# Optimization experiments

Measured on AMD Instinct MI355X. Metric: run time of the kernel, lower is better.

The kernel has to match this reference:

```python
import jax, jax.numpy as jnp
import numpy as np

# Dimensions (see shape_source): 192x192 images, 10 MC samples, 4 classes (3 fg), batch 16
B, S, CLS, H, W = 16, 10, 4, 192, 192
FG = CLS - 1
FSCALE = 3   # neighbor-count kernel
CSCALE = 3   # constraint-reward kernel
K = float(CSCALE * CSCALE)


def setup_inputs() -> dict:
    key = jax.random.key(0)
    k1, k2 = jax.random.split(key)
    logits = jax.random.normal(k1, (B, CLS, H, W), dtype=jnp.float32)
    preds = jax.nn.softmax(logits, axis=1)          # per-pixel class probabilities
    samples = jax.random.randint(k2, (B, S, H, W), 0, CLS, dtype=jnp.int32)  # sampled label maps
    return {"preds": preds, "samples": samples}


def _conv_ones(x, ksize):
    # x: [N, H, W]; all-ones ksize x ksize conv, SAME padding (== pad (k-1)/2 in torch)
    kern = jnp.ones((1, 1, ksize, ksize), x.dtype)
    y = jax.lax.conv_general_dilated(x[:, None], kern, (1, 1), 'SAME')
    return y[:, 0]


def _dilate8(m):
    # 3x3 max-pool == one step of 8-connectivity dilation (skimage full connectivity)
    return jax.lax.reduce_window(m, 0.0, jax.lax.max, (3, 3), (1, 1), 'SAME')


def _flood(fg, seed):
    # connected component of fg containing flat index `seed` (8-connectivity),
    # equivalent to skimage.flood_fill from the seed followed by == new_value
    m0 = jnp.zeros(fg.size, fg.dtype).at[seed].set(1.0).reshape(fg.shape) * fg
    def cond(st):
        return st[1]
    def body(st):
        m, _ = st
        d = _dilate8(m) * fg
        return d, jnp.any(d != m)
    m, _ = jax.lax.while_loop(cond, body, (m0, jnp.array(True)))
    return m


def _connectivity_rewards(samples):
    # samples: [B, S, H, W] int class maps -> rewards [B, S, H, W]
    cls_ids = jnp.arange(1, CLS)
    fg = (samples[:, :, None] == cls_ids[None, None, :, None, None]).astype(jnp.float32)  # [B,S,FG,H,W]
    fgf = fg.reshape(-1, H, W)                     # [B*S*FG, H, W]
    nb = _conv_ones(fgf, FSCALE) * fgf             # foreground neighbor counts
    seeds = jnp.argmax(nb.reshape(nb.shape[0], -1), axis=1)  # seed = max-neighbor pixel (first max)
    comp = jax.vmap(_flood)(fgf, seeds)            # largest-seeded connected component
    fc = _conv_ones(comp, CSCALE) * comp           # F_fg_neigbors
    reward = fc / K                                # soft reward
    per_c = reward - (fgf - comp)                  # + isolation penalty: -(fg - fill_connect)
    return per_c.reshape(B, S, FG, H, W).sum(axis=2)


def reference(preds, samples):
    rewards = _connectivity_rewards(samples)       # [B,S,H,W], constant wrt preds
    # prob of the sampled class at each pixel: preds[b, samples[b,s,h,w], h, w]
    probs = jnp.take_along_axis(
        jnp.broadcast_to(preds[:, None], (B, S, CLS, H, W)),
        samples[:, :, None].astype(jnp.int32), axis=2)[:, :, 0]
    # REINFORCE-style constraint loss: maximize reward-weighted log-prob
    loss = -(jnp.log(probs + 1e-8) * rewards).mean()
    return loss
```

## Files before the change

kernel.cpp:

```cpp
#include <hip/hip_runtime.h>
#include <stdint.h>

#define BB 16
#define SS 10
#define CLSN 4
#define FGN 3
#define HH 192
#define WW 192
#define NPIX (HH * WW)
#define WPR 3
#define NWORDS (HH * WPR)
#define NT 512
#define NW 8
#define CH (NWORDS / NW)

typedef unsigned long long u64;

#define FAD(a, b, c, s, cy)            \
    do {                               \
        u64 t_ = (a) ^ (b);            \
        (s) = t_ ^ (c);                \
        (cy) = ((a) & (b)) | (t_ & (c)); \
    } while (0)

#define SMEAR3(u0, u1, u2, s0, s1, s2)                          \
    do {                                                        \
        (s0) = (u0) | ((u0) << 1) | ((u0) >> 1) | ((u1) << 63); \
        (s1) = (u1) | ((u1) << 1) | ((u0) >> 63) | ((u1) >> 1) | ((u2) << 63); \
        (s2) = (u2) | ((u2) << 1) | ((u1) >> 63) | ((u2) >> 1); \
    } while (0)

__device__ __forceinline__ void plane9(const u64* bd, int k,
                                       u64& P0, u64& P1, u64& P2, u64& P3, u64& mid)
{
    const int r = k / WPR;
    const int wc = k - r * WPR;
    u64 rows[3][3];
#pragma unroll
    for (int di = 0; di < 3; ++di) {
        int rr = r + di - 1;
#pragma unroll
        for (int dj = 0; dj < 3; ++dj) {
            int ww = wc + dj - 1;
            rows[di][dj] = (rr >= 0 && rr < HH && ww >= 0 && ww < WPR)
                           ? bd[rr * WPR + ww] : 0ULL;
        }
    }
    mid = rows[1][1];
    u64 in[9];
#pragma unroll
    for (int i = 0; i < 3; ++i) {
        u64 m = rows[i][1], lf = rows[i][0], rg = rows[i][2];
        in[3 * i + 0] = m;
        in[3 * i + 1] = (m << 1) | (lf >> 63);
        in[3 * i + 2] = (m >> 1) | (rg << 63);
    }
    u64 s0a, c0a, s0b, c0b, s0c, c0c, c0d, s1a, c1a, c1b;
    FAD(in[0], in[1], in[2], s0a, c0a);
    FAD(in[3], in[4], in[5], s0b, c0b);
    FAD(in[6], in[7], in[8], s0c, c0c);
    FAD(s0a, s0b, s0c, P0, c0d);
    FAD(c0a, c0b, c0c, s1a, c1a);
    P1 = s1a ^ c0d;
    c1b = s1a & c0d;
    P2 = c1a ^ c1b;
    P3 = c1a & c1b;
}

__global__ __launch_bounds__(NT) void cc_loss_kernel(
    const float* __restrict__ preds,
    const int* __restrict__ samples,
    double* __restrict__ acc)
{
    __shared__ u64 fgw[NWORDS];
    __shared__ u64 compB[NWORDS];
    __shared__ unsigned int wkey[NW];
    __shared__ double wsum[NW];
    __shared__ unsigned int seedIdx;

    const int blk = blockIdx.x;
    const int c = 1 + blk / (BB * SS);
    const int pair = blk % (BB * SS);
    const int b = pair / SS;
    const int s = pair % SS;

    const int tid  = threadIdx.x;
    const int lane = tid & 63;
    const int wv   = tid >> 6;

    const int* smp = samples + (size_t)pair * NPIX;
    const float* pp = preds + ((size_t)b * CLSN + c) * NPIX;

    float facc = 0.0f;

    {
        const int base = wv * CH;
        for (int i = 0; i < CH; i += 6) {
            int v[6]; float pv[6];
#pragma unroll
            for (int j = 0; j < 6; ++j) {
                int pix = ((base + i + j) << 6) + lane;
                v[j]  = smp[pix];
                pv[j] = pp[pix];
            }
#pragma unroll
            for (int j = 0; j < 6; ++j) {
                u64 m = __ballot(v[j] == c);
                if (lane == 0) fgw[base + i + j] = m;
                float lp = __logf(pv[j] + 1e-8f);
                facc -= (v[j] == c) ? lp : 0.0f;
            }
        }
    }
    __syncthreads();

    {
        unsigned int bestkey = 0u;
        for (int k = tid; k < NWORDS; k += NT) {
            u64 P0, P1, P2, P3, mid;
            plane9(fgw, k, P0, P1, P2, P3, mid);
            if (mid) {
                u64 cand = mid, t;
                unsigned v = 0;
                t = cand & P3; if (t) { cand = t; v |= 8u; }
                t = cand & P2; if (t) { cand = t; v |= 4u; }
                t = cand & P1; if (t) { cand = t; v |= 2u; }
                t = cand & P0; if (t) { cand = t; v |= 1u; }
                unsigned pix = ((unsigned)k << 6) + (unsigned)(__ffsll(cand) - 1);
                unsigned key = (v << 16) | (36863u - pix);
                if (key > bestkey) bestkey = key;
            }
        }
#pragma unroll
        for (int off = 32; off > 0; off >>= 1) {
            unsigned int o = (unsigned int)__shfl_xor((int)bestkey, off, 64);
            if (o > bestkey) bestkey = o;
        }
        if (lane == 0) wkey[wv] = bestkey;
    }
    __syncthreads();
    if (tid == 0) {
        unsigned int kk = 0u;
#pragma unroll
        for (int i = 0; i < NW; ++i)
            if (wkey[i] > kk) kk = wkey[i];
        seedIdx = 36863u - (kk & 0xFFFFu);
    }
    __syncthreads();

    if (wv == 0) {
        const unsigned seed = seedIdx;
        u64 f[3][3], cc[3][3];
        const int rbase = 3 * lane;
#pragma unroll
        for (int j = 0; j < 3; ++j)
#pragma unroll
            for (int w = 0; w < 3; ++w) {
                f[j][w] = fgw[(rbase + j) * WPR + w];
                cc[j][w] = 0ULL;
            }
        {
            const int sr = seed / WW, sw = (seed % WW) >> 6, sb = seed & 63;
            if (sr / 3 == lane)
                cc[sr % 3][sw] = (1ULL << sb) & f[sr % 3][sw];
        }
        for (;;) {
            u64 bA0 = __shfl_up(cc[2][0], 1, 64);
            u64 bA1 = __shfl_up(cc[2][1], 1, 64);
            u64 bA2 = __shfl_up(cc[2][2], 1, 64);
            u64 tB0 = __shfl_down(cc[0][0], 1, 64);
            u64 tB1 = __shfl_down(cc[0][1], 1, 64);
            u64 tB2 = __shfl_down(cc[0][2], 1, 64);
            if (lane == 0)  { bA0 = bA1 = bA2 = 0ULL; }
            if (lane == 63) { tB0 = tB1 = tB2 = 0ULL; }

            u64 o00 = cc[0][0], o01 = cc[0][1], o02 = cc[0][2];
            u64 o10 = cc[1][0], o11 = cc[1][1], o12 = cc[1][2];
            u64 o20 = cc[2][0], o21 = cc[2][1], o22 = cc[2][2];

            u64 u0, u1, u2, s0, s1, s2;
            u0 = bA0 | cc[0][0] | cc[1][0]; u1 = bA1 | cc[0][1] | cc[1][1]; u2 = bA2 | cc[0][2] | cc[1][2];
            SMEAR3(u0, u1, u2, s0, s1, s2);
            cc[0][0] = s0 & f[0][0]; cc[0][1] = s1 & f[0][1]; cc[0][2] = s2 & f[0][2];

            u0 = cc[0][0] | cc[1][0] | cc[2][0]; u1 = cc[0][1] | cc[1][1] | cc[2][1]; u2 = cc[0][2] | cc[1][2] | cc[2][2];
            SMEAR3(u0, u1, u2, s0, s1, s2);
            cc[1][0] = s0 & f[1][0]; cc[1][1] = s1 & f[1][1]; cc[1][2] = s2 & f[1][2];

            u0 = cc[1][0] | cc[2][0] | tB0; u1 = cc[1][1] | cc[2][1] | tB1; u2 = cc[1][2] | cc[2][2] | tB2;
            SMEAR3(u0, u1, u2, s0, s1, s2);
            cc[2][0] = s0 & f[2][0]; cc[2][1] = s1 & f[2][1]; cc[2][2] = s2 & f[2][2];

            u0 = cc[0][0] | cc[1][0] | cc[2][0]; u1 = cc[0][1] | cc[1][1] | cc[2][1]; u2 = cc[0][2] | cc[1][2] | cc[2][2];
            SMEAR3(u0, u1, u2, s0, s1, s2);
            cc[1][0] = s0 & f[1][0]; cc[1][1] = s1 & f[1][1]; cc[1][2] = s2 & f[1][2];

            u0 = bA0 | cc[0][0] | cc[1][0]; u1 = bA1 | cc[0][1] | cc[1][1]; u2 = bA2 | cc[0][2] | cc[1][2];
            SMEAR3(u0, u1, u2, s0, s1, s2);
            cc[0][0] = s0 & f[0][0]; cc[0][1] = s1 & f[0][1]; cc[0][2] = s2 & f[0][2];

            u64 d = (cc[0][0] ^ o00) | (cc[0][1] ^ o01) | (cc[0][2] ^ o02)
                  | (cc[1][0] ^ o10) | (cc[1][1] ^ o11) | (cc[1][2] ^ o12)
                  | (cc[2][0] ^ o20) | (cc[2][1] ^ o21) | (cc[2][2] ^ o22);
            if (!__any(d != 0ULL)) break;
        }
#pragma unroll
        for (int j = 0; j < 3; ++j)
#pragma unroll
            for (int w = 0; w < 3; ++w)
                compB[(rbase + j) * WPR + w] = cc[j][w];
    }
    __syncthreads();

    {
        const int base = wv * CH;
        for (int k = base; k < base + CH; ++k) {
            u64 cw = compB[k];
            if (cw == 0ULL) continue;
            u64 P0, P1, P2, P3, mid;
            plane9(compB, k, P0, P1, P2, P3, mid);
            if ((cw >> lane) & 1ULL) {
                int cnt = (int)((P0 >> lane) & 1ULL)
                        | ((int)((P1 >> lane) & 1ULL) << 1)
                        | ((int)((P2 >> lane) & 1ULL) << 2)
                        | ((int)((P3 >> lane) & 1ULL) << 3);
                float lp = __logf(pp[(k << 6) + lane] + 1e-8f);
                facc += ((float)cnt * (1.0f / 9.0f) + 1.0f) * lp;
            }
        }
    }

#pragma unroll
    for (int off = 32; off > 0; off >>= 1)
        facc += __shfl_xor(facc, off, 64);
    if (lane == 0) wsum[wv] = (double)facc;
    __syncthreads();
    if (tid == 0) {
        double t = 0.0;
#pragma unroll
        for (int i = 0; i < NW; ++i) t += wsum[i];
        atomicAdd(acc, t);
    }
}

__global__ void finalize_kernel(const double* __restrict__ acc, float* __restrict__ out)
{
    if (threadIdx.x == 0 && blockIdx.x == 0)
        out[0] = (float)(-acc[0] / (double)((long long)BB * SS * NPIX));
}

extern "C" void kernel_launch(void* const* d_in, const int* in_sizes, int n_in,
                              void* d_out, int out_size, void* d_ws, size_t ws_size,
                              hipStream_t stream)
{
    const float* preds   = (const float*)d_in[0];
    const int*   samples = (const int*)d_in[1];
    double* acc = (double*)d_ws;

    hipMemsetAsync(acc, 0, sizeof(double), stream);
    hipLaunchKernelGGL(cc_loss_kernel, dim3(BB * SS * FGN), dim3(NT), 0, stream,
                       preds, samples, acc);
    hipLaunchKernelGGL(finalize_kernel, dim3(1), dim3(64), 0, stream,
                       acc, (float*)d_out);
}
```

Measured before the change: 51.19 us.

## Split into dense bitmask pass and single-wave component kernel

Splits the fused kernel into two. The first is a dense pass that reads each sample once, writes foreground bitmasks for all three classes to workspace, and accumulates the -log p term. The second runs one 64-thread block per task to pick the seed, flood-fill, and score only the nonzero component words. This removes the threefold re-read of samples and the idle waves during the serial flood fill, at the cost of a global round-trip for the bitmasks and an extra launch. It falls back to the old fused kernel if the workspace is too small.

Result: slower. 85.88 us (+67.8%).

```diff
diff --git a/kernel.cpp b/kernel.cpp
--- a/kernel.cpp
+++ b/kernel.cpp
@@ -10,9 +10,13 @@
 #define NPIX (HH * WW)
 #define WPR 3
 #define NWORDS (HH * WPR)
-#define NT 512
-#define NW 8
-#define CH (NWORDS / NW)
+#define NPAIR (BB * SS)
+#define NTASK (NPAIR * FGN)
+
+#define K1_BLOCKS 1440
+#define K1_THREADS 256
+#define K1_WAVES (K1_BLOCKS * 4)
+#define K1_CHUNK ((NPAIR * NWORDS) / K1_WAVES)
 
 typedef unsigned long long u64;
 
@@ -67,22 +71,199 @@
     P3 = c1a & c1b;
 }
 
-__global__ __launch_bounds__(NT) void cc_loss_kernel(
+__global__ __launch_bounds__(K1_THREADS) void k1_dense(
+    const float* __restrict__ preds,
+    const int* __restrict__ samples,
+    u64* __restrict__ fgAll,
+    double* __restrict__ acc)
+{
+    __shared__ double wsum[4];
+    const int tid  = threadIdx.x;
+    const int lane = tid & 63;
+    const int wv   = tid >> 6;
+    const int wid  = blockIdx.x * 4 + wv;
+
+    float facc = 0.0f;
+    const int base = wid * K1_CHUNK;
+#pragma unroll 4
+    for (int i = 0; i < K1_CHUNK; ++i) {
+        const int t = base + i;
+        const int pair = t / NWORDS;
+        const int word = t - pair * NWORDS;
+        const int b = pair / SS;
+        const int pix = (word << 6) + lane;
+        const int v = samples[(size_t)pair * NPIX + pix];
+        const float p = preds[((size_t)b * CLSN + v) * NPIX + pix];
+        u64 m1 = __ballot(v == 1);
+        u64 m2 = __ballot(v == 2);
+        u64 m3 = __ballot(v == 3);
+        if (lane == 0) {
+            fgAll[(size_t)(0 * NPAIR + pair) * NWORDS + word] = m1;
+            fgAll[(size_t)(1 * NPAIR + pair) * NWORDS + word] = m2;
+            fgAll[(size_t)(2 * NPAIR + pair) * NWORDS + word] = m3;
+        }
+        float lp = __logf(p + 1e-8f);
+        facc -= (v > 0) ? lp : 0.0f;
+    }
+#pragma unroll
+    for (int off = 32; off > 0; off >>= 1)
+        facc += __shfl_xor(facc, off, 64);
+    if (lane == 0) wsum[wv] = (double)facc;
+    __syncthreads();
+    if (tid == 0)
+        atomicAdd(acc, wsum[0] + wsum[1] + wsum[2] + wsum[3]);
+}
+
+__global__ __launch_bounds__(64) void k2_comp(
+    const float* __restrict__ preds,
+    const u64* __restrict__ fgAll,
+    double* __restrict__ acc)
+{
+    __shared__ u64 fgw[NWORDS];
+    __shared__ u64 cmp[NWORDS];
+
+    const int blk  = blockIdx.x;
+    const int c    = 1 + blk / NPAIR;
+    const int pair = blk % NPAIR;
+    const int b    = pair / SS;
+    const int lane = threadIdx.x;
+
+    const u64* fgsrc = fgAll + (size_t)blk * NWORDS;
+#pragma unroll
+    for (int i = 0; i < 9; ++i)
+        fgw[lane + 64 * i] = fgsrc[lane + 64 * i];
+    __syncthreads();
+
+    unsigned int bestkey = 0u;
+#pragma unroll
+    for (int i = 0; i < 9; ++i) {
+        const int k = lane + 64 * i;
+        u64 P0, P1, P2, P3, mid;
+        plane9(fgw, k, P0, P1, P2, P3, mid);
+        if (mid) {
+            u64 cand = mid, t;
+            unsigned v = 0;
+            t = cand & P3; if (t) { cand = t; v |= 8u; }
+            t = cand & P2; if (t) { cand = t; v |= 4u; }
+            t = cand & P1; if (t) { cand = t; v |= 2u; }
+            t = cand & P0; if (t) { cand = t; v |= 1u; }
+            unsigned pix = ((unsigned)k << 6) + (unsigned)(__ffsll(cand) - 1);
+            unsigned key = (v << 16) | (36863u - pix);
+            if (key > bestkey) bestkey = key;
+        }
+    }
+#pragma unroll
+    for (int off = 32; off > 0; off >>= 1) {
+        unsigned int o = (unsigned int)__shfl_xor((int)bestkey, off, 64);
+        if (o > bestkey) bestkey = o;
+    }
+    const unsigned seed = 36863u - (bestkey & 0xFFFFu);
+
+    u64 f[3][3], cc[3][3];
+#pragma unroll
+    for (int j = 0; j < 3; ++j)
+#pragma unroll
+        for (int w = 0; w < 3; ++w) {
+            f[j][w] = fgw[(3 * lane + j) * WPR + w];
+            cc[j][w] = 0ULL;
+        }
+    {
+        const int sr = (int)(seed / WW), sw = ((int)seed % WW) >> 6, sb = (int)seed & 63;
+        if (sr / 3 == lane)
+            cc[sr % 3][sw] = (1ULL << sb) & f[sr % 3][sw];
+    }
+    for (;;) {
+        u64 bA0 = __shfl_up(cc[2][0], 1, 64);
+        u64 bA1 = __shfl_up(cc[2][1], 1, 64);
+        u64 bA2 = __shfl_up(cc[2][2], 1, 64);
+        u64 tB0 = __shfl_down(cc[0][0], 1, 64);
+        u64 tB1 = __shfl_down(cc[0][1], 1, 64);
+        u64 tB2 = __shfl_down(cc[0][2], 1, 64);
+        if (lane == 0)  { bA0 = bA1 = bA2 = 0ULL; }
+        if (lane == 63) { tB0 = tB1 = tB2 = 0ULL; }
+
+        u64 o00 = cc[0][0], o01 = cc[0][1], o02 = cc[0][2];
+        u64 o10 = cc[1][0], o11 = cc[1][1], o12 = cc[1][2];
+        u64 o20 = cc[2][0], o21 = cc[2][1], o22 = cc[2][2];
+
+        u64 u0, u1, u2, s0, s1, s2;
+        u0 = bA0 | cc[0][0] | cc[1][0]; u1 = bA1 | cc[0][1] | cc[1][1]; u2 = bA2 | cc[0][2] | cc[1][2];
+        SMEAR3(u0, u1, u2, s0, s1, s2);
+        cc[0][0] = s0 & f[0][0]; cc[0][1] = s1 & f[0][1]; cc[0][2] = s2 & f[0][2];
+
+        u0 = cc[0][0] | cc[1][0] | cc[2][0]; u1 = cc[0][1] | cc[1][1] | cc[2][1]; u2 = cc[0][2] | cc[1][2] | cc[2][2];
+        SMEAR3(u0, u1, u2, s0, s1, s2);
+        cc[1][0] = s0 & f[1][0]; cc[1][1] = s1 & f[1][1]; cc[1][2] = s2 & f[1][2];
+
+        u0 = cc[1][0] | cc[2][0] | tB0; u1 = cc[1][1] | cc[2][1] | tB1; u2 = cc[1][2] | cc[2][2] | tB2;
+        SMEAR3(u0, u1, u2, s0, s1, s2);
+        cc[2][0] = s0 & f[2][0]; cc[2][1] = s1 & f[2][1]; cc[2][2] = s2 & f[2][2];
+
+        u0 = cc[0][0] | cc[1][0] | cc[2][0]; u1 = cc[0][1] | cc[1][1] | cc[2][1]; u2 = cc[0][2] | cc[1][2] | cc[2][2];
+        SMEAR3(u0, u1, u2, s0, s1, s2);
+        cc[1][0] = s0 & f[1][0]; cc[1][1] = s1 & f[1][1]; cc[1][2] = s2 & f[1][2];
+
+        u0 = bA0 | cc[0][0] | cc[1][0]; u1 = bA1 | cc[0][1] | cc[1][1]; u2 = bA2 | cc[0][2] | cc[1][2];
+        SMEAR3(u0, u1, u2, s0, s1, s2);
+        cc[0][0] = s0 & f[0][0]; cc[0][1] = s1 & f[0][1]; cc[0][2] = s2 & f[0][2];
+
+        u64 d = (cc[0][0] ^ o00) | (cc[0][1] ^ o01) | (cc[0][2] ^ o02)
+              | (cc[1][0] ^ o10) | (cc[1][1] ^ o11) | (cc[1][2] ^ o12)
+              | (cc[2][0] ^ o20) | (cc[2][1] ^ o21) | (cc[2][2] ^ o22);
+        if (!__any(d != 0ULL)) break;
+    }
+
+#pragma unroll
+    for (int j = 0; j < 3; ++j)
+#pragma unroll
+        for (int w = 0; w < 3; ++w)
+            cmp[(3 * lane + j) * WPR + w] = cc[j][w];
+    __syncthreads();
+
+    float facc = 0.0f;
+    const float* pp = preds + ((size_t)b * CLSN + c) * NPIX;
+#pragma unroll
+    for (int jw = 0; jw < 9; ++jw) {
+        const int j = jw / 3, w = jw - 3 * (jw / 3);
+        u64 m = __ballot(cc[j][w] != 0ULL);
+        while (m) {
+            const int src = (int)(__ffsll(m) - 1);
+            m &= m - 1;
+            const int k = 9 * src + jw;
+            u64 P0, P1, P2, P3, mid;
+            plane9(cmp, k, P0, P1, P2, P3, mid);
+            if ((mid >> lane) & 1ULL) {
+                int cnt = (int)((P0 >> lane) & 1ULL)
+                        | ((int)((P1 >> lane) & 1ULL) << 1)
+                        | ((int)((P2 >> lane) & 1ULL) << 2)
+                        | ((int)((P3 >> lane) & 1ULL) << 3);
+                float lp = __logf(pp[(k << 6) + lane] + 1e-8f);
+                facc += ((float)cnt * (1.0f / 9.0f) + 1.0f) * lp;
+            }
+        }
+    }
+#pragma unroll
+    for (int off = 32; off > 0; off >>= 1)
+        facc += __shfl_xor(facc, off, 64);
+    if (lane == 0)
+        atomicAdd(acc, (double)facc);
+}
+
+__global__ __launch_bounds__(512) void cc_loss_fused(
     const float* __restrict__ preds,
     const int* __restrict__ samples,
     double* __restrict__ acc)
 {
     __shared__ u64 fgw[NWORDS];
     __shared__ u64 compB[NWORDS];
-    __shared__ unsigned int wkey[NW];
-    __shared__ double wsum[NW];
+    __shared__ unsigned int wkey[8];
+    __shared__ double wsum[8];
     __shared__ unsigned int seedIdx;
 
     const int blk = blockIdx.x;
-    const int c = 1 + blk / (BB * SS);
-    const int pair = blk % (BB * SS);
+    const int c = 1 + blk / NPAIR;
+    const int pair = blk % NPAIR;
     const int b = pair / SS;
-    const int s = pair % SS;
 
     const int tid  = threadIdx.x;
     const int lane = tid & 63;
@@ -92,10 +273,9 @@
     const float* pp = preds + ((size_t)b * CLSN + c) * NPIX;
 
     float facc = 0.0f;
-
     {
-        const int base = wv * CH;
-        for (int i = 0; i < CH; i += 6) {
+        const int base = wv * 72;
+        for (int i = 0; i < 72; i += 6) {
             int v[6]; float pv[6];
 #pragma unroll
             for (int j = 0; j < 6; ++j) {
@@ -113,10 +293,9 @@
         }
     }
     __syncthreads();
-
     {
         unsigned int bestkey = 0u;
-        for (int k = tid; k < NWORDS; k += NT) {
+        for (int k = tid; k < NWORDS; k += 512) {
             u64 P0, P1, P2, P3, mid;
             plane9(fgw, k, P0, P1, P2, P3, mid);
             if (mid) {
@@ -142,12 +321,11 @@
     if (tid == 0) {
         unsigned int kk = 0u;
 #pragma unroll
-        for (int i = 0; i < NW; ++i)
+        for (int i = 0; i < 8; ++i)
             if (wkey[i] > kk) kk = wkey[i];
         seedIdx = 36863u - (kk & 0xFFFFu);
     }
     __syncthreads();
-
     if (wv == 0) {
         const unsigned seed = seedIdx;
         u64 f[3][3], cc[3][3];
@@ -173,32 +351,25 @@
             u64 tB2 = __shfl_down(cc[0][2], 1, 64);
             if (lane == 0)  { bA0 = bA1 = bA2 = 0ULL; }
             if (lane == 63) { tB0 = tB1 = tB2 = 0ULL; }
-
             u64 o00 = cc[0][0], o01 = cc[0][1], o02 = cc[0][2];
             u64 o10 = cc[1][0], o11 = cc[1][1], o12 = cc[1][2];
             u64 o20 = cc[2][0], o21 = cc[2][1], o22 = cc[2][2];
-
             u64 u0, u1, u2, s0, s1, s2;
             u0 = bA0 | cc[0][0] | cc[1][0]; u1 = bA1 | cc[0][1] | cc[1][1]; u2 = bA2 | cc[0][2] | cc[1][2];
             SMEAR3(u0, u1, u2, s0, s1, s2);
             cc[0][0] = s0 & f[0][0]; cc[0][1] = s1 & f[0][1]; cc[0][2] = s2 & f[0][2];
-
             u0 = cc[0][0] | cc[1][0] | cc[2][0]; u1 = cc[0][1] | cc[1][1] | cc[2][1]; u2 = cc[0][2] | cc[1][2] | cc[2][2];
             SMEAR3(u0, u1, u2, s0, s1, s2);
             cc[1][0] = s0 & f[1][0]; cc[1][1] = s1 & f[1][1]; cc[1][2] = s2 & f[1][2];
-
             u0 = cc[1][0] | cc[2][0] | tB0; u1 = cc[1][1] | cc[2][1] | tB1; u2 = cc[1][2] | cc[2][2] | tB2;
             SMEAR3(u0, u1, u2, s0, s1, s2);
             cc[2][0] = s0 & f[2][0]; cc[2][1] = s1 & f[2][1]; cc[2][2] = s2 & f[2][2];
-
             u0 = cc[0][0] | cc[1][0] | cc[2][0]; u1 = cc[0][1] | cc[1][1] | cc[2][1]; u2 = cc[0][2] | cc[1][2] | cc[2][2];
             SMEAR3(u0, u1, u2, s0, s1, s2);
             cc[1][0] = s0 & f[1][0]; cc[1][1] = s1 & f[1][1]; cc[1][2] = s2 & f[1][2];
-
             u0 = bA0 | cc[0][0] | cc[1][0]; u1 = bA1 | cc[0][1] | cc[1][1]; u2 = bA2 | cc[0][2] | cc[1][2];
             SMEAR3(u0, u1, u2, s0, s1, s2);
             cc[0][0] = s0 & f[0][0]; cc[0][1] = s1 & f[0][1]; cc[0][2] = s2 & f[0][2];
-
             u64 d = (cc[0][0] ^ o00) | (cc[0][1] ^ o01) | (cc[0][2] ^ o02)
                   | (cc[1][0] ^ o10) | (cc[1][1] ^ o11) | (cc[1][2] ^ o12)
                   | (cc[2][0] ^ o20) | (cc[2][1] ^ o21) | (cc[2][2] ^ o22);
@@ -211,10 +382,9 @@
                 compB[(rbase + j) * WPR + w] = cc[j][w];
     }
     __syncthreads();
-
     {
-        const int base = wv * CH;
-        for (int k = base; k < base + CH; ++k) {
+        const int base = wv * 72;
+        for (int k = base; k < base + 72; ++k) {
             u64 cw = compB[k];
             if (cw == 0ULL) continue;
             u64 P0, P1, P2, P3, mid;
@@ -229,7 +399,6 @@
             }
         }
     }
-
 #pragma unroll
     for (int off = 32; off > 0; off >>= 1)
         facc += __shfl_xor(facc, off, 64);
@@ -238,7 +407,7 @@
     if (tid == 0) {
         double t = 0.0;
 #pragma unroll
-        for (int i = 0; i < NW; ++i) t += wsum[i];
+        for (int i = 0; i < 8; ++i) t += wsum[i];
         atomicAdd(acc, t);
     }
 }
@@ -255,11 +424,24 @@
 {
     const float* preds   = (const float*)d_in[0];
     const int*   samples = (const int*)d_in[1];
-    double* acc = (double*)d_ws;
-
-    hipMemsetAsync(acc, 0, sizeof(double), stream);
-    hipLaunchKernelGGL(cc_loss_kernel, dim3(BB * SS * FGN), dim3(NT), 0, stream,
-                       preds, samples, acc);
-    hipLaunchKernelGGL(finalize_kernel, dim3(1), dim3(64), 0, stream,
-                       acc, (float*)d_out);
-}
+
+    const size_t fg_bytes = (size_t)NTASK * NWORDS * sizeof(u64);
+    if (ws_size >= fg_bytes + sizeof(double)) {
+        u64* fgAll  = (u64*)d_ws;
+        double* acc = (double*)((char*)d_ws + fg_bytes);
+        hipMemsetAsync(acc, 0, sizeof(double), stream);
+        hipLaunchKernelGGL(k1_dense, dim3(K1_BLOCKS), dim3(K1_THREADS), 0, stream,
+                           preds, samples, fgAll, acc);
+        hipLaunchKernelGGL(k2_comp, dim3(NTASK), dim3(64), 0, stream,
+                           preds, fgAll, acc);
+        hipLaunchKernelGGL(finalize_kernel, dim3(1), dim3(64), 0, stream,
+                           acc, (float*)d_out);
+    } else {
+        double* acc = (double*)d_ws;
+        hipMemsetAsync(acc, 0, sizeof(double), stream);
+        hipLaunchKernelGGL(cc_loss_fused, dim3(NTASK), dim3(512), 0, stream,
+                           preds, samples, acc);
+        hipLaunchKernelGGL(finalize_kernel, dim3(1), dim3(64), 0, stream,
+                           acc, (float*)d_out);
+    }
+}
```

## Vectorize mask build, double-step flood rows, compact nonzero component words

Applied to the files above, without the earlier changes.

Each thread now loads 16 contiguous pixels with int4/float4 loads and packs a 16-bit mask directly into shared memory, replacing the per-word ballots. The block size drops from 512 to 256 threads. Each flood-fill row step now smears twice per iteration so the fill converges in fewer loop iterations. The reward pass first compacts the nonzero component words into a list with shared atomics and then prefetches the next word's probabilities while computing the current one. Fewer threads per block means less parallelism for the load phase, and the compaction adds an extra synchronisation.

New measurement: 49.35 us. -3.6%, faster.

```diff
diff --git a/kernel.cpp b/kernel.cpp
--- a/kernel.cpp
+++ b/kernel.cpp
@@ -10,11 +10,13 @@
 #define NPIX (HH * WW)
 #define WPR 3
 #define NWORDS (HH * WPR)
-#define NT 512
-#define NW 8
-#define CH (NWORDS / NW)
+#define NPAIR (BB * SS)
+#define NTASK (NPAIR * FGN)
+#define NT 256
+#define NW 4
 
 typedef unsigned long long u64;
+typedef unsigned short u16;
 
 #define FAD(a, b, c, s, cy)            \
     do {                               \
@@ -67,55 +69,71 @@
     P3 = c1a & c1b;
 }
 
-__global__ __launch_bounds__(NT) void cc_loss_kernel(
+__global__ __launch_bounds__(NT) void cc_fused(
     const float* __restrict__ preds,
     const int* __restrict__ samples,
     double* __restrict__ acc)
 {
     __shared__ u64 fgw[NWORDS];
-    __shared__ u64 compB[NWORDS];
-    __shared__ unsigned int wkey[NW];
+    __shared__ u64 cmp[NWORDS];
+    __shared__ unsigned wkey[NW];
     __shared__ double wsum[NW];
-    __shared__ unsigned int seedIdx;
+    __shared__ unsigned seedSh;
+    __shared__ int cntSh;
+    __shared__ short wlist[NWORDS];
 
     const int blk = blockIdx.x;
-    const int c = 1 + blk / (BB * SS);
-    const int pair = blk % (BB * SS);
+    const int c = 1 + blk / NPAIR;
+    const int pair = blk % NPAIR;
     const int b = pair / SS;
-    const int s = pair % SS;
 
     const int tid  = threadIdx.x;
     const int lane = tid & 63;
     const int wv   = tid >> 6;
 
-    const int* smp = samples + (size_t)pair * NPIX;
-    const float* pp = preds + ((size_t)b * CLSN + c) * NPIX;
+    const int* __restrict__ smp  = samples + (size_t)pair * NPIX;
+    const float* __restrict__ pp = preds + ((size_t)b * CLSN + c) * NPIX;
+
+    if (tid == 0) cntSh = 0;
 
     float facc = 0.0f;
 
     {
-        const int base = wv * CH;
-        for (int i = 0; i < CH; i += 6) {
-            int v[6]; float pv[6];
-#pragma unroll
-            for (int j = 0; j < 6; ++j) {
-                int pix = ((base + i + j) << 6) + lane;
-                v[j]  = smp[pix];
-                pv[j] = pp[pix];
-            }
-#pragma unroll
-            for (int j = 0; j < 6; ++j) {
-                u64 m = __ballot(v[j] == c);
-                if (lane == 0) fgw[base + i + j] = m;
-                float lp = __logf(pv[j] + 1e-8f);
-                facc -= (v[j] == c) ? lp : 0.0f;
-            }
+        u16* nib = (u16*)fgw;
+        for (int sc = 0; sc < 9; ++sc) {
+            const int ci = sc * NT + tid;
+            const int px = ci << 4;
+            const int4 v0 = *(const int4*)(smp + px);
+            const int4 v1 = *(const int4*)(smp + px + 4);
+            const int4 v2 = *(const int4*)(smp + px + 8);
+            const int4 v3 = *(const int4*)(smp + px + 12);
+            const float4 q0 = *(const float4*)(pp + px);
+            const float4 q1 = *(const float4*)(pp + px + 4);
+            const float4 q2 = *(const float4*)(pp + px + 8);
+            const float4 q3 = *(const float4*)(pp + px + 12);
+            unsigned m = 0u;
+#define ACC1(vv, qq, sh)                                              \
+            {                                                          \
+                const bool hit_ = ((vv) == c);                         \
+                m |= ((unsigned)hit_) << (sh);                         \
+                facc -= hit_ ? __logf((qq) + 1e-8f) : 0.0f;            \
+            }
+            ACC1(v0.x, q0.x, 0)  ACC1(v0.y, q0.y, 1)
+            ACC1(v0.z, q0.z, 2)  ACC1(v0.w, q0.w, 3)
+            ACC1(v1.x, q1.x, 4)  ACC1(v1.y, q1.y, 5)
+            ACC1(v1.z, q1.z, 6)  ACC1(v1.w, q1.w, 7)
+            ACC1(v2.x, q2.x, 8)  ACC1(v2.y, q2.y, 9)
+            ACC1(v2.z, q2.z, 10) ACC1(v2.w, q2.w, 11)
+            ACC1(v3.x, q3.x, 12) ACC1(v3.y, q3.y, 13)
+            ACC1(v3.z, q3.z, 14) ACC1(v3.w, q3.w, 15)
+#undef ACC1
+            nib[ci] = (u16)m;
         }
     }
     __syncthreads();
 
     {
-        unsigned int bestkey = 0u;
+        unsigned bestkey = 0u;
         for (int k = tid; k < NWORDS; k += NT) {
             u64 P0, P1, P2, P3, mid;
             plane9(fgw, k, P0, P1, P2, P3, mid);
@@ -133,23 +151,23 @@
         }
 #pragma unroll
         for (int off = 32; off > 0; off >>= 1) {
-            unsigned int o = (unsigned int)__shfl_xor((int)bestkey, off, 64);
+            unsigned o = (unsigned)__shfl_xor((int)bestkey, off, 64);
             if (o > bestkey) bestkey = o;
         }
         if (lane == 0) wkey[wv] = bestkey;
     }
     __syncthreads();
     if (tid == 0) {
-        unsigned int kk = 0u;
-#pragma unroll
-        for (int i = 0; i < NW; ++i)
-            if (wkey[i] > kk) kk = wkey[i];
-        seedIdx = 36863u - (kk & 0xFFFFu);
+        unsigned kk = wkey[0];
+        if (wkey[1] > kk) kk = wkey[1];
+        if (wkey[2] > kk) kk = wkey[2];
+        if (wkey[3] > kk) kk = wkey[3];
+        seedSh = 36863u - (kk & 0xFFFFu);
     }
     __syncthreads();
 
     if (wv == 0) {
-        const unsigned seed = seedIdx;
+        const unsigned seed = seedSh;
         u64 f[3][3], cc[3][3];
         const int rbase = 3 * lane;
 #pragma unroll
@@ -160,7 +178,7 @@
                 cc[j][w] = 0ULL;
             }
         {
-            const int sr = seed / WW, sw = (seed % WW) >> 6, sb = seed & 63;
+            const int sr = (int)(seed / WW), sw = ((int)seed % WW) >> 6, sb = (int)seed & 63;
             if (sr / 3 == lane)
                 cc[sr % 3][sw] = (1ULL << sb) & f[sr % 3][sw];
         }
@@ -178,26 +196,25 @@
             u64 o10 = cc[1][0], o11 = cc[1][1], o12 = cc[1][2];
             u64 o20 = cc[2][0], o21 = cc[2][1], o22 = cc[2][2];
 
-            u64 u0, u1, u2, s0, s1, s2;
-            u0 = bA0 | cc[0][0] | cc[1][0]; u1 = bA1 | cc[0][1] | cc[1][1]; u2 = bA2 | cc[0][2] | cc[1][2];
-            SMEAR3(u0, u1, u2, s0, s1, s2);
-            cc[0][0] = s0 & f[0][0]; cc[0][1] = s1 & f[0][1]; cc[0][2] = s2 & f[0][2];
-
-            u0 = cc[0][0] | cc[1][0] | cc[2][0]; u1 = cc[0][1] | cc[1][1] | cc[2][1]; u2 = cc[0][2] | cc[1][2] | cc[2][2];
-            SMEAR3(u0, u1, u2, s0, s1, s2);
-            cc[1][0] = s0 & f[1][0]; cc[1][1] = s1 & f[1][1]; cc[1][2] = s2 & f[1][2];
-
-            u0 = cc[1][0] | cc[2][0] | tB0; u1 = cc[1][1] | cc[2][1] | tB1; u2 = cc[1][2] | cc[2][2] | tB2;
-            SMEAR3(u0, u1, u2, s0, s1, s2);
-            cc[2][0] = s0 & f[2][0]; cc[2][1] = s1 & f[2][1]; cc[2][2] = s2 & f[2][2];
-
-            u0 = cc[0][0] | cc[1][0] | cc[2][0]; u1 = cc[0][1] | cc[1][1] | cc[2][1]; u2 = cc[0][2] | cc[1][2] | cc[2][2];
-            SMEAR3(u0, u1, u2, s0, s1, s2);
-            cc[1][0] = s0 & f[1][0]; cc[1][1] = s1 & f[1][1]; cc[1][2] = s2 & f[1][2];
-
-            u0 = bA0 | cc[0][0] | cc[1][0]; u1 = bA1 | cc[0][1] | cc[1][1]; u2 = bA2 | cc[0][2] | cc[1][2];
-            SMEAR3(u0, u1, u2, s0, s1, s2);
-            cc[0][0] = s0 & f[0][0]; cc[0][1] = s1 & f[0][1]; cc[0][2] = s2 & f[0][2];
+#define RSTEP(A0, A1, A2, B0, B1, B2, C0, C1, C2, J)                          \
+            {                                                                  \
+                u64 u0 = (A0) | (B0) | (C0);                                   \
+                u64 u1 = (A1) | (B1) | (C1);                                   \
+                u64 u2 = (A2) | (B2) | (C2);                                   \
+                u64 t0, t1, t2, s0, s1, s2;                                    \
+                SMEAR3(u0, u1, u2, t0, t1, t2);                                \
+                t0 &= f[J][0]; t1 &= f[J][1]; t2 &= f[J][2];                   \
+                SMEAR3(t0, t1, t2, s0, s1, s2);                                \
+                cc[J][0] = s0 & f[J][0];                                       \
+                cc[J][1] = s1 & f[J][1];                                       \
+                cc[J][2] = s2 & f[J][2];                                       \
+            }
+            RSTEP(bA0, bA1, bA2, cc[0][0], cc[0][1], cc[0][2], cc[1][0], cc[1][1], cc[1][2], 0)
+            RSTEP(cc[0][0], cc[0][1], cc[0][2], cc[1][0], cc[1][1], cc[1][2], cc[2][0], cc[2][1], cc[2][2], 1)
+            RSTEP(cc[1][0], cc[1][1], cc[1][2], cc[2][0], cc[2][1], cc[2][2], tB0, tB1, tB2, 2)
+            RSTEP(cc[0][0], cc[0][1], cc[0][2], cc[1][0], cc[1][1], cc[1][2], cc[2][0], cc[2][1], cc[2][2], 1)
+            RSTEP(bA0, bA1, bA2, cc[0][0], cc[0][1], cc[0][2], cc[1][0], cc[1][1], cc[1][2], 0)
+#undef RSTEP
 
             u64 d = (cc[0][0] ^ o00) | (cc[0][1] ^ o01) | (cc[0][2] ^ o02)
                   | (cc[1][0] ^ o10) | (cc[1][1] ^ o11) | (cc[1][2] ^ o12)
@@ -208,25 +225,34 @@
         for (int j = 0; j < 3; ++j)
 #pragma unroll
             for (int w = 0; w < 3; ++w)
-                compB[(rbase + j) * WPR + w] = cc[j][w];
-    }
-    __syncthreads();
-
+                cmp[(rbase + j) * WPR + w] = cc[j][w];
+    }
+    __syncthreads();
+
+    for (int k = tid; k < NWORDS; k += NT)
+        if (cmp[k] != 0ULL) { int idx = atomicAdd(&cntSh, 1); wlist[idx] = (short)k; }
+    __syncthreads();
     {
-        const int base = wv * CH;
-        for (int k = base; k < base + CH; ++k) {
-            u64 cw = compB[k];
-            if (cw == 0ULL) continue;
+        const int n = cntSh;
+        int i = wv;
+        int kc = (i < n) ? (int)wlist[i] : -1;
+        float pc = 0.0f;
+        if (kc >= 0) pc = pp[(kc << 6) + lane];
+        while (kc >= 0) {
+            const int i2 = i + NW;
+            const int k2 = (i2 < n) ? (int)wlist[i2] : -1;
+            float p2 = 0.0f;
+            if (k2 >= 0) p2 = pp[(k2 << 6) + lane];
             u64 P0, P1, P2, P3, mid;
-            plane9(compB, k, P0, P1, P2, P3, mid);
-            if ((cw >> lane) & 1ULL) {
-                int cnt = (int)((P0 >> lane) & 1ULL)
-                        | ((int)((P1 >> lane) & 1ULL) << 1)
-                        | ((int)((P2 >> lane) & 1ULL) << 2)
-                        | ((int)((P3 >> lane) & 1ULL) << 3);
-                float lp = __logf(pp[(k << 6) + lane] + 1e-8f);
-                facc += ((float)cnt * (1.0f / 9.0f) + 1.0f) * lp;
-            }
+            plane9(cmp, kc, P0, P1, P2, P3, mid);
+            if ((mid >> lane) & 1ULL) {
+                int ct = (int)((P0 >> lane) & 1ULL)
+                       | ((int)((P1 >> lane) & 1ULL) << 1)
+                       | ((int)((P2 >> lane) & 1ULL) << 2)
+                       | ((int)((P3 >> lane) & 1ULL) << 3);
+                facc += ((float)ct * (1.0f / 9.0f) + 1.0f) * __logf(pc + 1e-8f);
+            }
+            i = i2; kc = k2; pc = p2;
         }
     }
 
@@ -235,12 +261,8 @@
         facc += __shfl_xor(facc, off, 64);
     if (lane == 0) wsum[wv] = (double)facc;
     __syncthreads();
-    if (tid == 0) {
-        double t = 0.0;
-#pragma unroll
-        for (int i = 0; i < NW; ++i) t += wsum[i];
-        atomicAdd(acc, t);
-    }
+    if (tid == 0)
+        atomicAdd(acc, wsum[0] + wsum[1] + wsum[2] + wsum[3]);
 }
 
 __global__ void finalize_kernel(const double* __restrict__ acc, float* __restrict__ out)
@@ -258,7 +280,7 @@
     double* acc = (double*)d_ws;
 
     hipMemsetAsync(acc, 0, sizeof(double), stream);
-    hipLaunchKernelGGL(cc_loss_kernel, dim3(BB * SS * FGN), dim3(NT), 0, stream,
+    hipLaunchKernelGGL(cc_fused, dim3(NTASK), dim3(NT), 0, stream,
                        preds, samples, acc);
     hipLaunchKernelGGL(finalize_kernel, dim3(1), dim3(64), 0, stream,
                        acc, (float*)d_out);
```
